# Kernel tuning notes

Measured on AMD Instinct MI355X. Metric: run time of the kernel, lower is better.

The kernel has to match this reference:

```python
import jax, jax.numpy as jnp
import numpy as np

B, D = 8, 256
MEM, CW, R, K, KL = 131072, 64, 4, 4, 4
C = R * K + 2 * KL + 1  # 25 visible cells
DELTA = 0.005
EPS = 1e-6
TIMESTEP = 1.0  # first step after reset


def _gather(x, idx):
    # x: (b,m) or (b,m,w); idx: (b,k)
    if x.ndim == 2:
        return jnp.take_along_axis(x, idx, axis=1)
    e = jnp.broadcast_to(idx[:, :, None], idx.shape + (x.shape[-1],))
    return jnp.take_along_axis(x, e, axis=1)


def _fwd(xi, memory, visible_memory, link_matrix, rev_link_matrix, precedence,
         read_weights, write_weights, usage,
         W_rq, b_rq, W_wv, b_wv, W_ig, b_ig, W_wg, b_wg,
         read_positions):
    b = xi.shape[0]
    bidx = jnp.arange(b)[:, None]

    # interface transforms (independent linears)
    read_query = (xi @ W_rq + b_rq).reshape(b, R, CW)      # (b,r,w)
    write_vector = (xi @ W_wv + b_wv).reshape(b, 1, CW)    # (b,1,w)
    ig = jax.nn.sigmoid(xi @ W_ig + b_ig)                  # (b,c)
    wg = jax.nn.sigmoid(xi @ W_wg + b_wg)                  # (b,1)

    # ------------------ write ------------------
    rw_vis = _gather(read_weights, read_positions)         # (b,c)
    ww_vis = _gather(write_weights, read_positions)        # (b,c)

    # usage update + least-used indicator over visible cells
    u = (rw_vis + ww_vis > DELTA).astype(memory.dtype)
    rel = _gather(usage, read_positions)
    I_min = (rel == jnp.min(rel, axis=-1, keepdims=True)).astype(memory.dtype)
    rel_new = (TIMESTEP - rel) * u + rel * (1.0 - u)
    usage = usage.at[bidx, read_positions].set(rel_new)

    # interpolated write weights over visible cells
    ww_new = wg * (ig * rw_vis + (1.0 - ig) * I_min)       # (b,c)
    write_weights = write_weights.at[bidx, read_positions].set(ww_new)

    # erase + write into visible memory, scatter back into sparse memory
    visible_memory = visible_memory * (1.0 - I_min[:, :, None]) + ww_new[:, :, None] * write_vector
    memory = memory.at[bidx, read_positions].set(visible_memory)

    # link matrix / reverse link matrix update
    trp = read_positions[:, R * K:R * K + 2 * KL]          # temporal positions (b,2KL)
    Ieye = jnp.eye(MEM, 2 * KL, dtype=memory.dtype)[None]  # eye(m,k) mask as in torch code
    prec_dense = jnp.zeros_like(write_weights).at[bidx, trp].set(precedence)  # (b,m)
    tww = _gather(write_weights, trp)                      # (b,2KL)
    link_matrix = ((1.0 - write_weights[:, :, None]) * link_matrix
                   + write_weights[:, :, None] * precedence[:, None, :]) * Ieye
    rev_link_matrix = ((1.0 - tww[:, None, :]) * rev_link_matrix
                       + tww[:, None, :] * prec_dense[:, :, None]) * Ieye

    # precedence update and least-used cell (argmin usage)
    precedence = (1.0 - jnp.sum(tww, axis=-1, keepdims=True)) * precedence + tww
    least_used = jax.lax.top_k(-usage, 1)[1]               # (b,1)

    # ------------------ read ------------------
    trw = _gather(read_weights, trp)                       # (b,2KL)
    fwd_w = jnp.einsum('bmk,bk->bm', link_matrix, trw)     # forward weighting
    bwd_w = jnp.einsum('bmk,bk->bm', rev_link_matrix, trw) # backward weighting

    # exact L2 k-NN over full memory (dense surrogate for the FAISS search)
    mem_sq = jnp.sum(memory * memory, axis=-1)             # (b,m)
    dots = jnp.einsum('brw,bmw->brm', read_query, memory)  # (b,r,m)
    knn = jax.lax.top_k(2.0 * dots - mem_sq[:, None, :], K)[1].reshape(b, R * K)

    fp = jax.lax.top_k(fwd_w, KL)[1]
    bp = jax.lax.top_k(bwd_w, KL)[1]
    lum = jnp.full((b, 1), C + 1, dtype=knn.dtype)         # timestep <= mem_size branch
    max_length = least_used[0, 0]                          # mem_limit_reached == False
    positions = jnp.clip(
        jnp.concatenate([knn, fp.astype(knn.dtype), bp.astype(knn.dtype), lum], axis=1),
        0, max_length)                                     # (b,c)

    visible = _gather(memory, positions)                   # (b,c,w)
    kq = read_query / (jnp.linalg.norm(read_query, axis=-1, keepdims=True) + EPS)
    vn = visible / (jnp.linalg.norm(visible, axis=-1, keepdims=True) + EPS)
    sim = jnp.einsum('brw,bcw->brc', kq, vn)               # cosine similarity
    rw_c = jax.nn.softmax(sim, axis=-1)                    # (b,r,c)
    read_vectors = jnp.einsum('brc,bcw->brw', rw_c, visible)
    return read_vectors


def setup_inputs() -> dict:
    key = jax.random.key(0)
    ks = jax.random.split(key, 16)
    inp = {}
    inp['xi'] = jax.random.normal(ks[0], (B, D), jnp.float32)
    inp['memory'] = jax.random.normal(ks[1], (B, MEM, CW), jnp.float32)
    inp['visible_memory'] = jax.random.normal(ks[2], (B, C, CW), jnp.float32)
    inp['link_matrix'] = 0.1 * jax.random.uniform(ks[3], (B, MEM, 2 * KL), jnp.float32)
    inp['rev_link_matrix'] = 0.1 * jax.random.uniform(ks[4], (B, MEM, 2 * KL), jnp.float32)
    inp['precedence'] = 0.1 * jax.random.uniform(ks[5], (B, 2 * KL), jnp.float32)
    inp['read_weights'] = 0.01 * jax.random.uniform(ks[6], (B, MEM), jnp.float32)
    inp['write_weights'] = 0.01 * jax.random.uniform(ks[7], (B, MEM), jnp.float32)
    usage = 0.5 + 0.5 * jax.random.uniform(ks[8], (B, MEM), jnp.float32)
    inp['usage'] = usage.at[:, MEM - 1].set(0.0)  # argmin lands at m-1 so the clamp is a no-op
    inp['least_used_mem'] = jnp.full((B, 1), MEM // 2, jnp.int32)
    inp['read_positions'] = jax.random.randint(ks[9], (B, C), 0, MEM)

    def lin(k, fi, fo):
        s = (6.0 / fi) ** 0.5  # kaiming-uniform-like
        return jax.random.uniform(k, (fi, fo), jnp.float32, -s, s)
    inp['W_rq'] = lin(ks[10], D, R * CW); inp['b_rq'] = jnp.zeros((R * CW,), jnp.float32)
    inp['W_wv'] = lin(ks[11], D, CW);     inp['b_wv'] = jnp.zeros((CW,), jnp.float32)
    inp['W_ig'] = lin(ks[12], D, C);      inp['b_ig'] = jnp.zeros((C,), jnp.float32)
    inp['W_wg'] = lin(ks[13], D, 1);      inp['b_wg'] = jnp.zeros((1,), jnp.float32)
    return inp


def reference(xi, memory, visible_memory, link_matrix, rev_link_matrix, precedence,
              read_weights, write_weights, usage, least_used_mem, read_positions,
              W_rq, b_rq, W_wv, b_wv, W_ig, b_ig, W_wg, b_wg):
    # least_used_mem is overwritten inside write() (argmin of updated usage) before use
    return _fwd(xi, memory, visible_memory, link_matrix, rev_link_matrix, precedence,
                read_weights, write_weights, usage,
                W_rq, b_rq, W_wv, b_wv, W_ig, b_ig, W_wg, b_wg,
                read_positions)
```

## Files before the change

kernel.cpp:

```cpp
#include <hip/hip_runtime.h>
#include <math.h>

#define BN 8
#define DDIM 256
#define MEMN 131072
#define CWN 64
#define RN 4
#define CN 25
#define DELTA_C 0.005f
#define EPS_C 1e-6f
#define RPB 1024
#define NBLK (MEMN / RPB)
#define NEG_INF (-3.402823466e38f)
#define IMAX 0x7fffffff


__device__ inline void wave_reduce_max(float& v, int& i, int& t) {
#pragma unroll
  for (int off = 32; off; off >>= 1) {
    float ov = __shfl_down(v, off);
    int oi = __shfl_down(i, off);
    int ot = __shfl_down(t, off);
    if (ov > v || (ov == v && oi < i)) { v = ov; i = oi; t = ot; }
  }
}

__device__ inline void block_argmax256(int tid, float v, int i, int t,
                                       float& rv, int& ri, int& rt) {
  __shared__ float sv[4];
  __shared__ int si[4], st[4];
  __shared__ float bv;
  __shared__ int bi, bt;
  wave_reduce_max(v, i, t);
  if ((tid & 63) == 0) { int w = tid >> 6; sv[w] = v; si[w] = i; st[w] = t; }
  __syncthreads();
  if (tid == 0) {
    float xv = sv[0]; int xi = si[0], xt = st[0];
#pragma unroll
    for (int w = 1; w < 4; w++)
      if (sv[w] > xv || (sv[w] == xv && si[w] < xi)) { xv = sv[w]; xi = si[w]; xt = st[w]; }
    bv = xv; bi = xi; bt = xt;
  }
  __syncthreads();
  rv = bv; ri = bi; rt = bt;
  __syncthreads();
}

__device__ inline void top4_of8(const float* v8, int* out4) {
  float val[12]; int idx[12]; bool used[12];
#pragma unroll
  for (int i = 0; i < 12; i++) { val[i] = (i < 8) ? v8[i] : 0.f; idx[i] = i; used[i] = false; }
  for (int r = 0; r < 4; r++) {
    int best = -1;
    for (int i = 0; i < 12; i++) {
      if (used[i]) continue;
      if (best < 0 || val[i] > val[best]) best = i;
    }
    used[best] = true;
    out4[r] = idx[best];
  }
}

__global__ __launch_bounds__(256) void k1_heads(
    const float* __restrict__ xi,
    const float* __restrict__ Wrq, const float* __restrict__ brq,
    const float* __restrict__ Wwv, const float* __restrict__ bwv,
    const float* __restrict__ Wig, const float* __restrict__ big,
    const float* __restrict__ Wwg, const float* __restrict__ bwg,
    float* rq, float* wv, float* ig, float* wg) {
  int b = blockIdx.x, tid = threadIdx.x;
  __shared__ float x[DDIM];
  x[tid] = xi[b * DDIM + tid];
  __syncthreads();
  {
    float s = brq[tid];
    for (int d = 0; d < DDIM; d++) s = fmaf(x[d], Wrq[d * 256 + tid], s);
    rq[b * 256 + tid] = s;
  }
  if (tid < 64) {
    float s = bwv[tid];
    for (int d = 0; d < DDIM; d++) s = fmaf(x[d], Wwv[d * 64 + tid], s);
    wv[b * 64 + tid] = s;
  } else if (tid < 64 + CN) {
    int o = tid - 64;
    float s = big[o];
    for (int d = 0; d < DDIM; d++) s = fmaf(x[d], Wig[d * CN + o], s);
    ig[b * CN + o] = 1.f / (1.f + expf(-s));
  } else if (tid == 64 + CN) {
    float s = bwg[0];
    for (int d = 0; d < DDIM; d++) s = fmaf(x[d], Wwg[d], s);
    wg[b] = 1.f / (1.f + expf(-s));
  }
}

__global__ __launch_bounds__(256) void k2_state(
    const float* __restrict__ vm, const float* __restrict__ prec,
    const float* __restrict__ rw, float* wwg, float* usage, float* memory,
    const float* __restrict__ lm, const float* __restrict__ rlm,
    const int* __restrict__ rp,
    const float* __restrict__ wv, const float* __restrict__ ig,
    const float* __restrict__ wg, int* fp, int* bp) {
  int b = blockIdx.x, tid = threadIdx.x;
  __shared__ int pos[CN];
  __shared__ float s_rw[CN], s_ww[CN], s_rel[CN], s_relnew[CN], s_imin[CN], s_wwnew[CN];
  __shared__ int s_guard[CN];
  __shared__ float minrel;
  __shared__ float fwd8[8], bwd8[8];

  if (tid < CN) {
    int p = rp[b * CN + tid];
    pos[tid] = p;
    s_rw[tid] = rw[(size_t)b * MEMN + p];
    s_ww[tid] = wwg[(size_t)b * MEMN + p];
    s_rel[tid] = usage[(size_t)b * MEMN + p];
  }
  __syncthreads();
  if (tid == 0) {
    float m = s_rel[0];
    for (int j = 1; j < CN; j++) m = fminf(m, s_rel[j]);
    minrel = m;
  }
  __syncthreads();
  if (tid < CN) {
    float u = (s_rw[tid] + s_ww[tid] > DELTA_C) ? 1.f : 0.f;
    float im = (s_rel[tid] == minrel) ? 1.f : 0.f;
    s_imin[tid] = im;
    s_relnew[tid] = u * (1.f - s_rel[tid]) + (1.f - u) * s_rel[tid];
    float igv = ig[b * CN + tid];
    s_wwnew[tid] = wg[b] * (igv * s_rw[tid] + (1.f - igv) * im);
    int g = 1;
    for (int j = tid + 1; j < CN; j++)
      if (pos[j] == pos[tid]) { g = 0; break; }
    s_guard[tid] = g;
  }
  __syncthreads();
  if (tid < CN && s_guard[tid]) {
    usage[(size_t)b * MEMN + pos[tid]] = s_relnew[tid];
    wwg[(size_t)b * MEMN + pos[tid]] = s_wwnew[tid];
  }
  for (int it = 0; it < 7; it++) {
    int j = it * 4 + (tid >> 6);
    int lane = tid & 63;
    if (j < CN && s_guard[j]) {
      float v = vm[((size_t)b * CN + j) * 64 + lane] * (1.f - s_imin[j]) +
                s_wwnew[j] * wv[b * 64 + lane];
      memory[((size_t)b * MEMN + pos[j]) * 64 + lane] = v;
    }
  }
  __syncthreads();
  if (tid < 8) {
    int m = tid;
    int trp_m = pos[16 + m];
    float tww = 0.f;
    for (int j = CN - 1; j >= 0; j--)
      if (pos[j] == trp_m) { tww = s_wwnew[j]; break; }
    float trw = rw[(size_t)b * MEMN + trp_m];
    float wwu;
    {
      int found = -1;
      for (int j = CN - 1; j >= 0; j--)
        if (pos[j] == m) { found = j; break; }
      wwu = (found >= 0) ? s_wwnew[found] : wwg[(size_t)b * MEMN + m];
    }
    float lmd = (1.f - wwu) * lm[((size_t)b * MEMN + m) * 8 + m] + wwu * prec[b * 8 + m];
    float pd = 0.f;
    for (int k = 7; k >= 0; k--)
      if (pos[16 + k] == m) { pd = prec[b * 8 + k]; break; }
    float rld = (1.f - tww) * rlm[((size_t)b * MEMN + m) * 8 + m] + tww * pd;
    fwd8[m] = lmd * trw;
    bwd8[m] = rld * trw;
  }
  __syncthreads();
  if (tid == 0) top4_of8(fwd8, &fp[b * 4]);
  if (tid == 1) top4_of8(bwd8, &bp[b * 4]);
}

__global__ __launch_bounds__(256) void k3_scan(
    const float* __restrict__ memory, const float* __restrict__ usage,
    const float* __restrict__ rq,
    float* blk_sv, int* blk_si, float* blk_uv, int* blk_ui) {
  int tid = threadIdx.x;
  int b = blockIdx.x / NBLK;
  int blk = blockIdx.x % NBLK;
  int base = blk * RPB;
  __shared__ float q[4][64];
  q[tid >> 6][tid & 63] = rq[b * 256 + tid];
  __syncthreads();

  float cs[4][4];
  int ci[4][4];
#pragma unroll
  for (int r = 0; r < 4; r++)
#pragma unroll
    for (int j = 0; j < 4; j++) { cs[r][j] = NEG_INF; ci[r][j] = IMAX; }
  float uvneg = NEG_INF;
  int ui = IMAX;

  const float4* q0 = (const float4*)(&q[0][0]);
  const float4* q1 = (const float4*)(&q[1][0]);
  const float4* q2 = (const float4*)(&q[2][0]);
  const float4* q3 = (const float4*)(&q[3][0]);

#pragma unroll
  for (int rr = 0; rr < RPB / 256; rr++) {
    int m = base + rr * 256 + tid;
    const float4* row4 = (const float4*)(memory + ((size_t)b * MEMN + m) * 64);
    float ds[4] = {0.f, 0.f, 0.f, 0.f};
    float sq = 0.f;
#pragma unroll
    for (int k = 0; k < 16; k++) {
      float4 x = row4[k];
      float4 a0 = q0[k], a1 = q1[k], a2 = q2[k], a3 = q3[k];
      ds[0] = fmaf(x.x, a0.x, fmaf(x.y, a0.y, fmaf(x.z, a0.z, fmaf(x.w, a0.w, ds[0]))));
      ds[1] = fmaf(x.x, a1.x, fmaf(x.y, a1.y, fmaf(x.z, a1.z, fmaf(x.w, a1.w, ds[1]))));
      ds[2] = fmaf(x.x, a2.x, fmaf(x.y, a2.y, fmaf(x.z, a2.z, fmaf(x.w, a2.w, ds[2]))));
      ds[3] = fmaf(x.x, a3.x, fmaf(x.y, a3.y, fmaf(x.z, a3.z, fmaf(x.w, a3.w, ds[3]))));
      sq = fmaf(x.x, x.x, fmaf(x.y, x.y, fmaf(x.z, x.z, fmaf(x.w, x.w, sq))));
    }
#pragma unroll
    for (int r = 0; r < 4; r++) {
      float s = 2.f * ds[r] - sq;
      if (s > cs[r][3] || (s == cs[r][3] && m < ci[r][3])) {
        cs[r][3] = s; ci[r][3] = m;
#define CSWAP(a, bq)                                                            \
        if (cs[r][a] > cs[r][bq] || (cs[r][a] == cs[r][bq] && ci[r][a] < ci[r][bq])) { \
          float tv = cs[r][a]; cs[r][a] = cs[r][bq]; cs[r][bq] = tv;            \
          int ti = ci[r][a]; ci[r][a] = ci[r][bq]; ci[r][bq] = ti; }
        CSWAP(3, 2)
        CSWAP(2, 1)
        CSWAP(1, 0)
#undef CSWAP
      }
    }
    float u = usage[(size_t)b * MEMN + m];
    float nu = -u;
    if (nu > uvneg || (nu == uvneg && m < ui)) { uvneg = nu; ui = m; }
  }

#pragma unroll
  for (int r = 0; r < 4; r++) {
    for (int round = 0; round < 4; round++) {
      float rvv; int rii, rtt;
      block_argmax256(tid, cs[r][0], ci[r][0], tid, rvv, rii, rtt);
      if (tid == 0) {
        size_t o = (((size_t)b * 4 + r) * NBLK + blk) * 4 + round;
        blk_sv[o] = rvv;
        blk_si[o] = rii;
      }
      if (tid == rtt) {
        cs[r][0] = cs[r][1]; ci[r][0] = ci[r][1];
        cs[r][1] = cs[r][2]; ci[r][1] = ci[r][2];
        cs[r][2] = cs[r][3]; ci[r][2] = ci[r][3];
        cs[r][3] = NEG_INF; ci[r][3] = IMAX;
      }
    }
  }
  {
    float rvv; int rii, rtt;
    block_argmax256(tid, uvneg, ui, tid, rvv, rii, rtt);
    if (tid == 0) {
      blk_uv[b * NBLK + blk] = -rvv;
      blk_ui[b * NBLK + blk] = rii;
    }
  }
}

__global__ __launch_bounds__(256) void k4_merge(
    const float* __restrict__ blk_sv, const int* __restrict__ blk_si,
    const float* __restrict__ blk_uv, const int* __restrict__ blk_ui,
    int* knn, int* least) {
  int b = blockIdx.x, tid = threadIdx.x;
  for (int r = 0; r < 4; r++) {
    size_t o = (size_t)(b * 4 + r) * NBLK * 4;
    float v0 = blk_sv[o + 2 * tid], v1 = blk_sv[o + 2 * tid + 1];
    int i0 = blk_si[o + 2 * tid], i1 = blk_si[o + 2 * tid + 1];
    if (v1 > v0 || (v1 == v0 && i1 < i0)) {
      float tv = v0; v0 = v1; v1 = tv;
      int ti = i0; i0 = i1; i1 = ti;
    }
    for (int round = 0; round < 4; round++) {
      float rvv; int rii, rtt;
      block_argmax256(tid, v0, i0, tid, rvv, rii, rtt);
      if (tid == 0) knn[b * 16 + r * 4 + round] = rii;
      if (tid == rtt) { v0 = v1; i0 = i1; v1 = NEG_INF; i1 = IMAX; }
    }
  }
  float uv = (tid < NBLK) ? -blk_uv[b * NBLK + tid] : NEG_INF;
  int uidx = (tid < NBLK) ? blk_ui[b * NBLK + tid] : IMAX;
  float rvv; int rii, rtt;
  block_argmax256(tid, uv, uidx, tid, rvv, rii, rtt);
  if (tid == 0) least[b] = rii;
}

__global__ __launch_bounds__(256) void k5_attn(
    const float* __restrict__ memory, const float* __restrict__ rq,
    const int* __restrict__ knn, const int* __restrict__ fp,
    const int* __restrict__ bp, const int* __restrict__ least,
    float* out) {
  int b = blockIdx.x, tid = threadIdx.x;
  __shared__ int pos[CN];
  __shared__ float vis[CN][64];
  __shared__ float vnorm[CN];
  __shared__ float rnorm[4];
  __shared__ float sim[4][CN];
  __shared__ float pw[4][CN];
  __shared__ float qs[4][64];
  int L = least[0];
  if (tid < CN) {
    int v;
    if (tid < 16) v = knn[b * 16 + tid];
    else if (tid < 20) v = fp[b * 4 + tid - 16];
    else if (tid < 24) v = bp[b * 4 + tid - 20];
    else v = CN + 1;
    v = min(v, L);
    v = max(v, 0);
    pos[tid] = v;
  }
  qs[tid >> 6][tid & 63] = rq[b * 256 + tid];
  __syncthreads();
  for (int it = 0; it < 7; it++) {
    int j = it * 4 + (tid >> 6);
    int lane = tid & 63;
    if (j < CN) vis[j][lane] = memory[((size_t)b * MEMN + pos[j]) * 64 + lane];
  }
  __syncthreads();
  if (tid < CN) {
    float s = 0.f;
    for (int k = 0; k < 64; k++) s = fmaf(vis[tid][k], vis[tid][k], s);
    vnorm[tid] = sqrtf(s) + EPS_C;
  }
  if (tid >= 32 && tid < 36) {
    int r = tid - 32;
    float s = 0.f;
    for (int k = 0; k < 64; k++) s = fmaf(qs[r][k], qs[r][k], s);
    rnorm[r] = sqrtf(s) + EPS_C;
  }
  __syncthreads();
  if (tid < 4 * CN) {
    int r = tid / CN, c = tid % CN;
    float s = 0.f;
    for (int k = 0; k < 64; k++) s = fmaf(qs[r][k], vis[c][k], s);
    sim[r][c] = s / (rnorm[r] * vnorm[c]);
  }
  __syncthreads();
  if (tid < 4) {
    int r = tid;
    float mx = NEG_INF;
    for (int c = 0; c < CN; c++) mx = fmaxf(mx, sim[r][c]);
    float sum = 0.f;
    for (int c = 0; c < CN; c++) { float e = expf(sim[r][c] - mx); pw[r][c] = e; sum += e; }
    float inv = 1.f / sum;
    for (int c = 0; c < CN; c++) pw[r][c] *= inv;
  }
  __syncthreads();
  {
    int r = tid >> 6, w = tid & 63;
    float s = 0.f;
    for (int c = 0; c < CN; c++) s = fmaf(pw[r][c], vis[c][w], s);
    out[(size_t)b * 256 + tid] = s;
  }
}

extern "C" void kernel_launch(void* const* d_in, const int* in_sizes, int n_in,
                              void* d_out, int out_size, void* d_ws, size_t ws_size,
                              hipStream_t stream) {
  const float* xi = (const float*)d_in[0];
  float* memory = (float*)d_in[1];
  const float* vm = (const float*)d_in[2];
  const float* lm = (const float*)d_in[3];
  const float* rlm = (const float*)d_in[4];
  const float* prec = (const float*)d_in[5];
  const float* rw = (const float*)d_in[6];
  float* wwg = (float*)d_in[7];
  float* usage = (float*)d_in[8];
  const int* rp = (const int*)d_in[10];
  const float* Wrq = (const float*)d_in[11];
  const float* brq = (const float*)d_in[12];
  const float* Wwv = (const float*)d_in[13];
  const float* bwv = (const float*)d_in[14];
  const float* Wig = (const float*)d_in[15];
  const float* big = (const float*)d_in[16];
  const float* Wwg = (const float*)d_in[17];
  const float* bwg = (const float*)d_in[18];
  float* out = (float*)d_out;

  float* f = (float*)d_ws;
  float* rq_w = f;   f += BN * 256;
  float* wv_w = f;   f += BN * 64;
  float* ig_w = f;   f += BN * CN;
  float* wg_w = f;   f += BN;
  float* blk_sv = f; f += (size_t)BN * 4 * NBLK * 4;
  float* blk_uv = f; f += BN * NBLK;
  int* ip = (int*)f;
  int* fp_w = ip;    ip += BN * 4;
  int* bp_w = ip;    ip += BN * 4;
  int* knn_w = ip;   ip += BN * 16;
  int* least_w = ip; ip += BN;
  int* blk_si = ip;  ip += (size_t)BN * 4 * NBLK * 4;
  int* blk_ui = ip;  ip += BN * NBLK;

  hipLaunchKernelGGL(k1_heads, dim3(BN), dim3(256), 0, stream,
                     xi, Wrq, brq, Wwv, bwv, Wig, big, Wwg, bwg,
                     rq_w, wv_w, ig_w, wg_w);
  hipLaunchKernelGGL(k2_state, dim3(BN), dim3(256), 0, stream,
                     vm, prec, rw, wwg, usage, memory, lm, rlm, rp,
                     wv_w, ig_w, wg_w, fp_w, bp_w);
  hipLaunchKernelGGL(k3_scan, dim3(BN * NBLK), dim3(256), 0, stream,
                     memory, usage, rq_w, blk_sv, blk_si, blk_uv, blk_ui);
  hipLaunchKernelGGL(k4_merge, dim3(BN), dim3(256), 0, stream,
                     blk_sv, blk_si, blk_uv, blk_ui, knn_w, least_w);
  hipLaunchKernelGGL(k5_attn, dim3(BN), dim3(256), 0, stream,
                     memory, rq_w, knn_w, fp_w, bp_w, least_w, out);
}
```

Before: 561.0 us.

## Restructure memory scan to coalesced 16-lane row dot products with shuffle reductions

The scan kernel now has each group of 16 lanes read one memory row cooperatively as float4s. This replaces the old pattern of one thread per row striding through 256 bytes, which gave poor coalescing, and the dot products are summed with xor shuffles. The per-block top-4 merge now goes through shared memory and 4 serial threads instead of 16 block-wide argmax reductions, and usage min uses vectorized float4 loads. The head linears also get unroll pragmas. The insertion into each lane's top-4 list no longer breaks ties by index, and the serial 64-element merge adds latency on a few threads.

```diff
diff --git a/kernel.cpp b/kernel.cpp
--- a/kernel.cpp
+++ b/kernel.cpp
@@ -74,20 +74,24 @@
   __syncthreads();
   {
     float s = brq[tid];
+#pragma unroll 8
     for (int d = 0; d < DDIM; d++) s = fmaf(x[d], Wrq[d * 256 + tid], s);
     rq[b * 256 + tid] = s;
   }
   if (tid < 64) {
     float s = bwv[tid];
+#pragma unroll 8
     for (int d = 0; d < DDIM; d++) s = fmaf(x[d], Wwv[d * 64 + tid], s);
     wv[b * 64 + tid] = s;
   } else if (tid < 64 + CN) {
     int o = tid - 64;
     float s = big[o];
+#pragma unroll 8
     for (int d = 0; d < DDIM; d++) s = fmaf(x[d], Wig[d * CN + o], s);
     ig[b * CN + o] = 1.f / (1.f + expf(-s));
   } else if (tid == 64 + CN) {
     float s = bwg[0];
+#pragma unroll 8
     for (int d = 0; d < DDIM; d++) s = fmaf(x[d], Wwg[d], s);
     wg[b] = 1.f / (1.f + expf(-s));
   }
@@ -183,81 +187,89 @@
   int b = blockIdx.x / NBLK;
   int blk = blockIdx.x % NBLK;
   int base = blk * RPB;
-  __shared__ float q[4][64];
-  q[tid >> 6][tid & 63] = rq[b * 256 + tid];
-  __syncthreads();
-
-  float cs[4][4];
-  int ci[4][4];
+  int wave = tid >> 6, lane = tid & 63;
+  int sub = lane & 15;
+  int grp = lane >> 4;
+
+  const float4* q4 = (const float4*)(rq + b * 256);
+  float4 qf0 = q4[0 * 16 + sub];
+  float4 qf1 = q4[1 * 16 + sub];
+  float4 qf2 = q4[2 * 16 + sub];
+  float4 qf3 = q4[3 * 16 + sub];
+
+  float tv0 = NEG_INF, tv1 = NEG_INF, tv2 = NEG_INF, tv3 = NEG_INF;
+  int ti0 = IMAX, ti1 = IMAX, ti2 = IMAX, ti3 = IMAX;
+
+  int rowbase = base + wave * 256;
+  const float4* mp = (const float4*)memory;
+  size_t lanebase = ((size_t)b * MEMN + rowbase) * 16 + (size_t)grp * 16 + sub;
+
+#pragma unroll 4
+  for (int it = 0; it < 64; it++) {
+    int m = rowbase + it * 4 + grp;
+    float4 x = mp[lanebase + (size_t)it * 64];
+    float d0 = fmaf(x.x, qf0.x, fmaf(x.y, qf0.y, fmaf(x.z, qf0.z, x.w * qf0.w)));
+    float d1 = fmaf(x.x, qf1.x, fmaf(x.y, qf1.y, fmaf(x.z, qf1.z, x.w * qf1.w)));
+    float d2 = fmaf(x.x, qf2.x, fmaf(x.y, qf2.y, fmaf(x.z, qf2.z, x.w * qf2.w)));
+    float d3 = fmaf(x.x, qf3.x, fmaf(x.y, qf3.y, fmaf(x.z, qf3.z, x.w * qf3.w)));
+    float sq = fmaf(x.x, x.x, fmaf(x.y, x.y, fmaf(x.z, x.z, x.w * x.w)));
 #pragma unroll
-  for (int r = 0; r < 4; r++)
-#pragma unroll
-    for (int j = 0; j < 4; j++) { cs[r][j] = NEG_INF; ci[r][j] = IMAX; }
-  float uvneg = NEG_INF;
-  int ui = IMAX;
-
-  const float4* q0 = (const float4*)(&q[0][0]);
-  const float4* q1 = (const float4*)(&q[1][0]);
-  const float4* q2 = (const float4*)(&q[2][0]);
-  const float4* q3 = (const float4*)(&q[3][0]);
-
-#pragma unroll
-  for (int rr = 0; rr < RPB / 256; rr++) {
-    int m = base + rr * 256 + tid;
-    const float4* row4 = (const float4*)(memory + ((size_t)b * MEMN + m) * 64);
-    float ds[4] = {0.f, 0.f, 0.f, 0.f};
-    float sq = 0.f;
-#pragma unroll
-    for (int k = 0; k < 16; k++) {
-      float4 x = row4[k];
-      float4 a0 = q0[k], a1 = q1[k], a2 = q2[k], a3 = q3[k];
-      ds[0] = fmaf(x.x, a0.x, fmaf(x.y, a0.y, fmaf(x.z, a0.z, fmaf(x.w, a0.w, ds[0]))));
-      ds[1] = fmaf(x.x, a1.x, fmaf(x.y, a1.y, fmaf(x.z, a1.z, fmaf(x.w, a1.w, ds[1]))));
-      ds[2] = fmaf(x.x, a2.x, fmaf(x.y, a2.y, fmaf(x.z, a2.z, fmaf(x.w, a2.w, ds[2]))));
-      ds[3] = fmaf(x.x, a3.x, fmaf(x.y, a3.y, fmaf(x.z, a3.z, fmaf(x.w, a3.w, ds[3]))));
-      sq = fmaf(x.x, x.x, fmaf(x.y, x.y, fmaf(x.z, x.z, fmaf(x.w, x.w, sq))));
-    }
-#pragma unroll
-    for (int r = 0; r < 4; r++) {
-      float s = 2.f * ds[r] - sq;
-      if (s > cs[r][3] || (s == cs[r][3] && m < ci[r][3])) {
-        cs[r][3] = s; ci[r][3] = m;
-#define CSWAP(a, bq)                                                            \
-        if (cs[r][a] > cs[r][bq] || (cs[r][a] == cs[r][bq] && ci[r][a] < ci[r][bq])) { \
-          float tv = cs[r][a]; cs[r][a] = cs[r][bq]; cs[r][bq] = tv;            \
-          int ti = ci[r][a]; ci[r][a] = ci[r][bq]; ci[r][bq] = ti; }
-        CSWAP(3, 2)
-        CSWAP(2, 1)
-        CSWAP(1, 0)
-#undef CSWAP
+    for (int off = 1; off < 16; off <<= 1) {
+      d0 += __shfl_xor(d0, off);
+      d1 += __shfl_xor(d1, off);
+      d2 += __shfl_xor(d2, off);
+      d3 += __shfl_xor(d3, off);
+      sq += __shfl_xor(sq, off);
+    }
+    float d = (sub == 0) ? d0 : (sub == 1) ? d1 : (sub == 2) ? d2 : d3;
+    float s = 2.f * d - sq;
+    if (sub < 4) {
+      if (s > tv3) {
+        tv3 = s; ti3 = m;
+        if (tv3 > tv2) { float t = tv2; tv2 = tv3; tv3 = t; int u = ti2; ti2 = ti3; ti3 = u; }
+        if (tv2 > tv1) { float t = tv1; tv1 = tv2; tv2 = t; int u = ti1; ti1 = ti2; ti2 = u; }
+        if (tv1 > tv0) { float t = tv0; tv0 = tv1; tv1 = t; int u = ti0; ti0 = ti1; ti1 = u; }
       }
     }
-    float u = usage[(size_t)b * MEMN + m];
-    float nu = -u;
-    if (nu > uvneg || (nu == uvneg && m < ui)) { uvneg = nu; ui = m; }
-  }
-
-#pragma unroll
-  for (int r = 0; r < 4; r++) {
+  }
+
+  __shared__ float lsv[4][16][4];
+  __shared__ int lsi[4][16][4];
+  if (sub < 4) {
+    int slot = wave * 4 + grp;
+    lsv[sub][slot][0] = tv0; lsi[sub][slot][0] = ti0;
+    lsv[sub][slot][1] = tv1; lsi[sub][slot][1] = ti1;
+    lsv[sub][slot][2] = tv2; lsi[sub][slot][2] = ti2;
+    lsv[sub][slot][3] = tv3; lsi[sub][slot][3] = ti3;
+  }
+  __syncthreads();
+  if (tid < 4) {
+    int r = tid;
+    size_t o = (((size_t)b * 4 + r) * NBLK + blk) * 4;
     for (int round = 0; round < 4; round++) {
-      float rvv; int rii, rtt;
-      block_argmax256(tid, cs[r][0], ci[r][0], tid, rvv, rii, rtt);
-      if (tid == 0) {
-        size_t o = (((size_t)b * 4 + r) * NBLK + blk) * 4 + round;
-        blk_sv[o] = rvv;
-        blk_si[o] = rii;
+      float bv = NEG_INF; int bi = IMAX; int bslot = 0, bj = 0;
+      for (int e = 0; e < 64; e++) {
+        int sl = e >> 2, j = e & 3;
+        float v = lsv[r][sl][j];
+        int ix = lsi[r][sl][j];
+        if (v > bv || (v == bv && ix < bi)) { bv = v; bi = ix; bslot = sl; bj = j; }
       }
-      if (tid == rtt) {
-        cs[r][0] = cs[r][1]; ci[r][0] = ci[r][1];
-        cs[r][1] = cs[r][2]; ci[r][1] = ci[r][2];
-        cs[r][2] = cs[r][3]; ci[r][2] = ci[r][3];
-        cs[r][3] = NEG_INF; ci[r][3] = IMAX;
-      }
-    }
-  }
+      lsv[r][bslot][bj] = NEG_INF;
+      blk_sv[o + round] = bv;
+      blk_si[o + round] = bi;
+    }
+  }
+
   {
+    const float4* u4 = (const float4*)(usage + (size_t)b * MEMN + base);
+    float4 uu = u4[tid];
+    int mb = base + tid * 4;
+    float uv = uu.x; int uix = mb;
+    if (uu.y < uv) { uv = uu.y; uix = mb + 1; }
+    if (uu.z < uv) { uv = uu.z; uix = mb + 2; }
+    if (uu.w < uv) { uv = uu.w; uix = mb + 3; }
     float rvv; int rii, rtt;
-    block_argmax256(tid, uvneg, ui, tid, rvv, rii, rtt);
+    block_argmax256(tid, -uv, uix, tid, rvv, rii, rtt);
     if (tid == 0) {
       blk_uv[b * NBLK + blk] = -rvv;
       blk_ui[b * NBLK + blk] = rii;
```

Result: faster. 524.5 us (-6.5%).
